# Performance work log

Hardware: AMD Instinct MI355X
Metric: run time of the kernel (lower is better)

The kernel has to match this reference:

```python
import jax, jax.numpy as jnp
import numpy as np

BETA = 0.25  # commitment loss weight


def setup_inputs() -> dict:
    key = jax.random.key(0)
    k1, k2 = jax.random.split(key)
    x = jax.random.normal(k1, (64, 64, 64, 64), dtype=jnp.float32)
    # embeddings: [embedding_dim=64, num_embeddings=512], random_uniform init in [-0.05, 0.05]
    embeddings = jax.random.uniform(k2, (64, 512), dtype=jnp.float32, minval=-0.05, maxval=0.05)
    return {"x": x, "embeddings": embeddings}


def reference(x, embeddings):
    d = embeddings.shape[0]
    flat = x.reshape(-1, d)                                   # [N, D]
    # squared L2 distances to each code: ||z||^2 + ||e||^2 - 2 z.e
    sim = flat @ embeddings                                   # [N, K]
    dist = (jnp.sum(flat * flat, axis=1, keepdims=True)
            + jnp.sum(embeddings * embeddings, axis=0)
            - 2.0 * sim)                                      # [N, K]
    idx = jnp.argmin(dist, axis=1)                            # [N]
    # gather nearest code (equivalent to one_hot @ embeddings.T)
    quantized = jnp.take(embeddings.T, idx, axis=0).reshape(x.shape)
    commitment_loss = jnp.mean((jax.lax.stop_gradient(quantized) - x) ** 2)
    codebook_loss = jnp.mean((quantized - jax.lax.stop_gradient(x)) ** 2)
    loss = BETA * commitment_loss + codebook_loss
    # straight-through estimator
    quantized_st = x + jax.lax.stop_gradient(quantized - x)
    return quantized_st, loss
```

## Files before the change

### kernel.cpp

```cpp
#include <hip/hip_runtime.h>


#define NROWS 262144
#define D 64
#define K 512
#define MARGIN 0.09f
#define INF32 3.4e38f

#define WS_ET 0
#define WS_E2 131072
#define WS_EBT 133120
#define WS_PARTIALS 198656

typedef __attribute__((ext_vector_type(8))) short bf16x8;
typedef __attribute__((ext_vector_type(4))) float f32x4;

union ClRed { unsigned cl[2048]; double red[256]; };

__device__ inline unsigned short f2bf(float f) {
    unsigned u = __float_as_uint(f);
    u += 0x7fffu + ((u >> 16) & 1u);
    return (unsigned short)(u >> 16);
}
__device__ inline unsigned pack_bf2(float lo, float hi) {
    unsigned ulo = __float_as_uint(lo); ulo += 0x7fffu + ((ulo >> 16) & 1u);
    unsigned uhi = __float_as_uint(hi); uhi += 0x7fffu + ((uhi >> 16) & 1u);
    return (ulo >> 16) | (uhi & 0xffff0000u);
}
__device__ inline bf16x8 pack8(float4 p, float4 q) {
    union { unsigned u[4]; bf16x8 v; } r;
    r.u[0] = pack_bf2(p.x, p.y); r.u[1] = pack_bf2(p.z, p.w);
    r.u[2] = pack_bf2(q.x, q.y); r.u[3] = pack_bf2(q.z, q.w);
    return r.v;
}

__global__ void __launch_bounds__(64) vq_prep(const float* __restrict__ emb, char* ws) {
    float* e2 = (float*)(ws + WS_E2);
    float* et = (float*)(ws + WS_ET);
    unsigned short* ebT = (unsigned short*)(ws + WS_EBT);
    int k = blockIdx.x * 64 + threadIdx.x;
    float v0 = emb[k];
    et[k * D] = v0;
    ebT[k * D] = f2bf(v0);
    float s = __fmul_rn(v0, v0);
    for (int d = 1; d < D; ++d) {
        float v = emb[d * K + k];
        et[k * D + d] = v;
        ebT[k * D + d] = f2bf(v);
        s = __fadd_rn(s, __fmul_rn(v, v));
    }
    e2[k] = s;
}

__device__ __noinline__ unsigned long long exact_pack(
        const float* __restrict__ x, const float* __restrict__ et,
        const float* __restrict__ e2f, int row, int k) {
    const float* xr = x + (size_t)row * D;
    float r0 = __fmul_rn(xr[0], xr[0]), r1 = __fmul_rn(xr[1], xr[1]);
    float r2 = __fmul_rn(xr[2], xr[2]), r3 = __fmul_rn(xr[3], xr[3]);
    float r4 = __fmul_rn(xr[4], xr[4]), r5 = __fmul_rn(xr[5], xr[5]);
    float r6 = __fmul_rn(xr[6], xr[6]), r7 = __fmul_rn(xr[7], xr[7]);
    for (int i = 8; i < 64; i += 8) {
        r0 = __fadd_rn(r0, __fmul_rn(xr[i],     xr[i]));
        r1 = __fadd_rn(r1, __fmul_rn(xr[i + 1], xr[i + 1]));
        r2 = __fadd_rn(r2, __fmul_rn(xr[i + 2], xr[i + 2]));
        r3 = __fadd_rn(r3, __fmul_rn(xr[i + 3], xr[i + 3]));
        r4 = __fadd_rn(r4, __fmul_rn(xr[i + 4], xr[i + 4]));
        r5 = __fadd_rn(r5, __fmul_rn(xr[i + 5], xr[i + 5]));
        r6 = __fadd_rn(r6, __fmul_rn(xr[i + 6], xr[i + 6]));
        r7 = __fadd_rn(r7, __fmul_rn(xr[i + 7], xr[i + 7]));
    }
    float z2 = __fadd_rn(__fadd_rn(__fadd_rn(r0, r1), __fadd_rn(r2, r3)),
                         __fadd_rn(__fadd_rn(r4, r5), __fadd_rn(r6, r7)));
    const float* ep = et + (size_t)k * D;
    float a = 0.f;
    for (int d = 0; d < D; ++d) a = fmaf(xr[d], ep[d], a);
    float dist = __fsub_rn(__fadd_rn(z2, e2f[k]), __fmul_rn(2.0f, a));
    return ((unsigned long long)__float_as_uint(dist) << 32) | (unsigned)k;
}

__global__ void __launch_bounds__(256) vq_fused(const float* __restrict__ x,
                                                float* __restrict__ out,
                                                char* __restrict__ ws) {
    const float* et  = (const float*)(ws + WS_ET);
    const float* e2f = (const float*)(ws + WS_E2);
    const unsigned short* ebT = (const unsigned short*)(ws + WS_EBT);
    double* partials = (double*)(ws + WS_PARTIALS);

    __shared__ unsigned short ebs[16384];
    __shared__ float le2[512];
    __shared__ unsigned long long lgmin[256];
    __shared__ int ccnt;
    __shared__ ClRed u;

    const int tid = threadIdx.x;
    const int wv = tid >> 6, lane = tid & 63;
    const int c15 = lane & 15;
    const int g = lane >> 4;
    const int kofs = g * 8;
    const int gr4 = g * 4;
    const int blockRow0 = blockIdx.x * 256;
    const int rowBase = blockRow0 + wv * 64;

    lgmin[tid] = 0xFFFFFFFFFFFFFFFFULL;
    if (tid == 0) ccnt = 0;
    le2[tid] = e2f[tid];
    le2[tid + 256] = e2f[tid + 256];

    bf16x8 aA0, aA1, aB0, aB1, aC0, aC1, aD0, aD1;
#define LOADA(RT, A0, A1) { \
    const float* xp = x + ((size_t)(rowBase + (RT) * 16 + c15)) * D + kofs; \
    float4 p0 = *(const float4*)xp; \
    float4 p1 = *(const float4*)(xp + 4); \
    float4 p2 = *(const float4*)(xp + 32); \
    float4 p3 = *(const float4*)(xp + 36); \
    A0 = pack8(p0, p1); A1 = pack8(p2, p3); }
    LOADA(0, aA0, aA1) LOADA(1, aB0, aB1) LOADA(2, aC0, aC1) LOADA(3, aD0, aD1)
#undef LOADA

#define STAGE(h) { \
    const uint4* src = (const uint4*)(ebT + (size_t)(h) * 16384); \
    _Pragma("unroll") \
    for (int i = 0; i < 8; ++i) { \
        int c = i * 256 + tid; \
        int kl = c >> 3, s = c & 7; \
        uint4 v = src[c]; \
        *(uint4*)(ebs + kl * 64 + ((s ^ (kl & 7)) * 8)) = v; \
    } }

#define SW1(A0, A1, M0, M1, M2, M3) { \
    f32x4 acc = {0.f, 0.f, 0.f, 0.f}; \
    acc = __builtin_amdgcn_mfma_f32_16x16x32_bf16(A0, bb0, acc, 0, 0, 0); \
    acc = __builtin_amdgcn_mfma_f32_16x16x32_bf16(A1, bb1, acc, 0, 0, 0); \
    M0 = fminf(M0, e2c - 2.0f * acc[0]); \
    M1 = fminf(M1, e2c - 2.0f * acc[1]); \
    M2 = fminf(M2, e2c - 2.0f * acc[2]); \
    M3 = fminf(M3, e2c - 2.0f * acc[3]); }

    float m00 = INF32, m01 = INF32, m02 = INF32, m03 = INF32;
    float m10 = INF32, m11 = INF32, m12 = INF32, m13 = INF32;
    float m20 = INF32, m21 = INF32, m22 = INF32, m23 = INF32;
    float m30 = INF32, m31 = INF32, m32 = INF32, m33 = INF32;

    for (int h = 0; h < 2; ++h) {
        __syncthreads();
        STAGE(h)
        __syncthreads();
        for (int j = 0; j < 16; ++j) {
            const int kkl = j * 16 + c15;
            bf16x8 bb0 = *(const bf16x8*)(ebs + kkl * 64 + ((g ^ (kkl & 7)) * 8));
            bf16x8 bb1 = *(const bf16x8*)(ebs + kkl * 64 + (((g + 4) ^ (kkl & 7)) * 8));
            float e2c = le2[h * 256 + kkl];
            SW1(aA0, aA1, m00, m01, m02, m03)
            SW1(aB0, aB1, m10, m11, m12, m13)
            SW1(aC0, aC1, m20, m21, m22, m23)
            SW1(aD0, aD1, m30, m31, m32, m33)
        }
    }
#undef SW1

#define RED(v) v = fminf(v, __shfl_xor(v, 1)); v = fminf(v, __shfl_xor(v, 2)); \
               v = fminf(v, __shfl_xor(v, 4)); v = fminf(v, __shfl_xor(v, 8)); \
               v += MARGIN;
    RED(m00) RED(m01) RED(m02) RED(m03)
    RED(m10) RED(m11) RED(m12) RED(m13)
    RED(m20) RED(m21) RED(m22) RED(m23)
    RED(m30) RED(m31) RED(m32) RED(m33)
#undef RED

#define PUSH(RT, R) { int idx = atomicAdd(&ccnt, 1); \
    if (idx < 2048) u.cl[idx] = \
        ((unsigned)(wv * 64 + (RT) * 16 + gr4 + (R)) << 16) | (unsigned)kg; \
    else atomicMin(&lgmin[wv * 64 + (RT) * 16 + gr4 + (R)], \
        exact_pack(x, et, e2f, blockRow0 + wv * 64 + (RT) * 16 + gr4 + (R), kg)); }

#define SW2(RT, A0, A1, M0, M1, M2, M3) { \
    f32x4 acc = {0.f, 0.f, 0.f, 0.f}; \
    acc = __builtin_amdgcn_mfma_f32_16x16x32_bf16(A0, bb0, acc, 0, 0, 0); \
    acc = __builtin_amdgcn_mfma_f32_16x16x32_bf16(A1, bb1, acc, 0, 0, 0); \
    if (e2c - 2.0f * acc[0] <= M0) PUSH(RT, 0) \
    if (e2c - 2.0f * acc[1] <= M1) PUSH(RT, 1) \
    if (e2c - 2.0f * acc[2] <= M2) PUSH(RT, 2) \
    if (e2c - 2.0f * acc[3] <= M3) PUSH(RT, 3) }

    for (int h = 0; h < 2; ++h) {
        __syncthreads();
        STAGE(h)
        __syncthreads();
        for (int j = 0; j < 16; ++j) {
            const int kkl = j * 16 + c15;
            const int kg = h * 256 + kkl;
            bf16x8 bb0 = *(const bf16x8*)(ebs + kkl * 64 + ((g ^ (kkl & 7)) * 8));
            bf16x8 bb1 = *(const bf16x8*)(ebs + kkl * 64 + (((g + 4) ^ (kkl & 7)) * 8));
            float e2c = le2[kg];
            SW2(0, aA0, aA1, m00, m01, m02, m03)
            SW2(1, aB0, aB1, m10, m11, m12, m13)
            SW2(2, aC0, aC1, m20, m21, m22, m23)
            SW2(3, aD0, aD1, m30, m31, m32, m33)
        }
    }
#undef SW2
#undef PUSH
#undef STAGE

    __syncthreads();
    const int cnt = (ccnt < 2048) ? ccnt : 2048;
    for (int i = tid; i < cnt; i += 256) {
        unsigned e = u.cl[i];
        int rowLocal = (int)(e >> 16);
        int k = (int)(e & 0x1ffu);
        atomicMin(&lgmin[rowLocal], exact_pack(x, et, e2f, blockRow0 + rowLocal, k));
    }
    __syncthreads();

    const int row = blockRow0 + tid;
    const int kb = (int)(lgmin[tid] & 0xFFFFFFFFULL);
    const float4* cq = (const float4*)(et + (size_t)kb * D);
    const float4* xr = (const float4*)(x + (size_t)row * D);
    float4* outr = (float4*)(out + (size_t)row * D);
    double rs = 0.0;
#define OUTQ(G) { \
        float4 e4 = cq[G]; float4 xv = xr[G]; float4 o; \
        float d0 = __fsub_rn(e4.x, xv.x); \
        float d1 = __fsub_rn(e4.y, xv.y); \
        float d2 = __fsub_rn(e4.z, xv.z); \
        float d3 = __fsub_rn(e4.w, xv.w); \
        o.x = __fadd_rn(xv.x, d0); \
        o.y = __fadd_rn(xv.y, d1); \
        o.z = __fadd_rn(xv.z, d2); \
        o.w = __fadd_rn(xv.w, d3); \
        outr[G] = o; \
        rs += (double)__fmul_rn(d0, d0) + (double)__fmul_rn(d1, d1) + \
              (double)__fmul_rn(d2, d2) + (double)__fmul_rn(d3, d3); }
    OUTQ(0) OUTQ(1) OUTQ(2) OUTQ(3) OUTQ(4) OUTQ(5) OUTQ(6) OUTQ(7)
    OUTQ(8) OUTQ(9) OUTQ(10) OUTQ(11) OUTQ(12) OUTQ(13) OUTQ(14) OUTQ(15)
#undef OUTQ

    u.red[tid] = rs;
    __syncthreads();
    for (int s = 128; s > 0; s >>= 1) {
        if (tid < s) u.red[tid] += u.red[tid + s];
        __syncthreads();
    }
    if (tid == 0) partials[blockIdx.x] = u.red[0];
}

__global__ void __launch_bounds__(256) vq_finalize(float* __restrict__ out, char* ws) {
    const double* partials = (const double*)(ws + WS_PARTIALS);
    __shared__ double red[256];
    double s = partials[threadIdx.x] + partials[threadIdx.x + 256] +
               partials[threadIdx.x + 512] + partials[threadIdx.x + 768];
    red[threadIdx.x] = s;
    __syncthreads();
    for (int st = 128; st > 0; st >>= 1) {
        if (threadIdx.x < st) red[threadIdx.x] += red[threadIdx.x + st];
        __syncthreads();
    }
    if (threadIdx.x == 0) {
        out[16777216] = (float)(1.25 * red[0] / 16777216.0);
    }
}

extern "C" void kernel_launch(void* const* d_in, const int* in_sizes, int n_in,
                              void* d_out, int out_size, void* d_ws, size_t ws_size,
                              hipStream_t stream) {
    const float* x   = (const float*)d_in[0];
    const float* emb = (const float*)d_in[1];
    float* out = (float*)d_out;
    char* ws = (char*)d_ws;

    vq_prep<<<8, 64, 0, stream>>>(emb, ws);
    vq_fused<<<NROWS / 256, 256, 0, stream>>>(x, out, ws);
    vq_finalize<<<1, 256, 0, stream>>>(out, ws);
}
```

Before: 183.7 us.

## Use single-wave blocks reading bf16 codebook directly from global/L2 instead of LDS staging

Shrinks the fused kernel from 256-thread to 64-thread blocks (one wavefront per block, 4096 blocks). The per-block LDS staging of the bf16 codebook and its barriers are removed, and each lane loads its B fragments straight from the global transposed codebook, relying on L1/L2 caching. The candidate list shrinks to 1024 entries and the loss partial sum becomes a shuffle reduction, with finalize summing 16 partials per thread. This removes LDS staging and block-wide syncs but adds global-memory latency to the inner MFMA loop, reads the codebook twice per wave, and increases the number of partials.

```diff
diff --git a/kernel.cpp b/kernel.cpp
--- a/kernel.cpp
+++ b/kernel.cpp
@@ -14,8 +14,6 @@
 
 typedef __attribute__((ext_vector_type(8))) short bf16x8;
 typedef __attribute__((ext_vector_type(4))) float f32x4;
-
-union ClRed { unsigned cl[2048]; double red[256]; };
 
 __device__ inline unsigned short f2bf(float f) {
     unsigned u = __float_as_uint(f);
@@ -79,33 +77,30 @@
     return ((unsigned long long)__float_as_uint(dist) << 32) | (unsigned)k;
 }
 
-__global__ void __launch_bounds__(256) vq_fused(const float* __restrict__ x,
-                                                float* __restrict__ out,
-                                                char* __restrict__ ws) {
+__global__ void __launch_bounds__(64, 4) vq_fused(const float* __restrict__ x,
+                                                  float* __restrict__ out,
+                                                  char* __restrict__ ws) {
     const float* et  = (const float*)(ws + WS_ET);
     const float* e2f = (const float*)(ws + WS_E2);
     const unsigned short* ebT = (const unsigned short*)(ws + WS_EBT);
     double* partials = (double*)(ws + WS_PARTIALS);
 
-    __shared__ unsigned short ebs[16384];
     __shared__ float le2[512];
-    __shared__ unsigned long long lgmin[256];
+    __shared__ unsigned long long lgmin[64];
+    __shared__ unsigned cl[1024];
     __shared__ int ccnt;
-    __shared__ ClRed u;
-
-    const int tid = threadIdx.x;
-    const int wv = tid >> 6, lane = tid & 63;
+
+    const int lane = threadIdx.x;
     const int c15 = lane & 15;
     const int g = lane >> 4;
     const int kofs = g * 8;
     const int gr4 = g * 4;
-    const int blockRow0 = blockIdx.x * 256;
-    const int rowBase = blockRow0 + wv * 64;
-
-    lgmin[tid] = 0xFFFFFFFFFFFFFFFFULL;
-    if (tid == 0) ccnt = 0;
-    le2[tid] = e2f[tid];
-    le2[tid + 256] = e2f[tid + 256];
+    const int rowBase = blockIdx.x * 64;
+
+    lgmin[lane] = 0xFFFFFFFFFFFFFFFFULL;
+    if (lane == 0) ccnt = 0;
+#pragma unroll
+    for (int i = 0; i < 8; ++i) le2[i * 64 + lane] = e2f[i * 64 + lane];
 
     bf16x8 aA0, aA1, aB0, aB1, aC0, aC1, aD0, aD1;
 #define LOADA(RT, A0, A1) { \
@@ -118,44 +113,32 @@
     LOADA(0, aA0, aA1) LOADA(1, aB0, aB1) LOADA(2, aC0, aC1) LOADA(3, aD0, aD1)
 #undef LOADA
 
-#define STAGE(h) { \
-    const uint4* src = (const uint4*)(ebT + (size_t)(h) * 16384); \
-    _Pragma("unroll") \
-    for (int i = 0; i < 8; ++i) { \
-        int c = i * 256 + tid; \
-        int kl = c >> 3, s = c & 7; \
-        uint4 v = src[c]; \
-        *(uint4*)(ebs + kl * 64 + ((s ^ (kl & 7)) * 8)) = v; \
-    } }
+    __syncthreads();
+
+    float m00 = INF32, m01 = INF32, m02 = INF32, m03 = INF32;
+    float m10 = INF32, m11 = INF32, m12 = INF32, m13 = INF32;
+    float m20 = INF32, m21 = INF32, m22 = INF32, m23 = INF32;
+    float m30 = INF32, m31 = INF32, m32 = INF32, m33 = INF32;
 
 #define SW1(A0, A1, M0, M1, M2, M3) { \
     f32x4 acc = {0.f, 0.f, 0.f, 0.f}; \
     acc = __builtin_amdgcn_mfma_f32_16x16x32_bf16(A0, bb0, acc, 0, 0, 0); \
     acc = __builtin_amdgcn_mfma_f32_16x16x32_bf16(A1, bb1, acc, 0, 0, 0); \
-    M0 = fminf(M0, e2c - 2.0f * acc[0]); \
-    M1 = fminf(M1, e2c - 2.0f * acc[1]); \
-    M2 = fminf(M2, e2c - 2.0f * acc[2]); \
-    M3 = fminf(M3, e2c - 2.0f * acc[3]); }
-
-    float m00 = INF32, m01 = INF32, m02 = INF32, m03 = INF32;
-    float m10 = INF32, m11 = INF32, m12 = INF32, m13 = INF32;
-    float m20 = INF32, m21 = INF32, m22 = INF32, m23 = INF32;
-    float m30 = INF32, m31 = INF32, m32 = INF32, m33 = INF32;
-
-    for (int h = 0; h < 2; ++h) {
-        __syncthreads();
-        STAGE(h)
-        __syncthreads();
-        for (int j = 0; j < 16; ++j) {
-            const int kkl = j * 16 + c15;
-            bf16x8 bb0 = *(const bf16x8*)(ebs + kkl * 64 + ((g ^ (kkl & 7)) * 8));
-            bf16x8 bb1 = *(const bf16x8*)(ebs + kkl * 64 + (((g + 4) ^ (kkl & 7)) * 8));
-            float e2c = le2[h * 256 + kkl];
-            SW1(aA0, aA1, m00, m01, m02, m03)
-            SW1(aB0, aB1, m10, m11, m12, m13)
-            SW1(aC0, aC1, m20, m21, m22, m23)
-            SW1(aD0, aD1, m30, m31, m32, m33)
-        }
+    M0 = fminf(M0, fmaf(-2.0f, acc[0], e2c)); \
+    M1 = fminf(M1, fmaf(-2.0f, acc[1], e2c)); \
+    M2 = fminf(M2, fmaf(-2.0f, acc[2], e2c)); \
+    M3 = fminf(M3, fmaf(-2.0f, acc[3], e2c)); }
+
+    for (int j = 0; j < 32; ++j) {
+        const int kkl = j * 16 + c15;
+        const unsigned short* bp = ebT + ((size_t)kkl << 6) + kofs;
+        bf16x8 bb0 = *(const bf16x8*)bp;
+        bf16x8 bb1 = *(const bf16x8*)(bp + 32);
+        float e2c = le2[kkl];
+        SW1(aA0, aA1, m00, m01, m02, m03)
+        SW1(aB0, aB1, m10, m11, m12, m13)
+        SW1(aC0, aC1, m20, m21, m22, m23)
+        SW1(aD0, aD1, m30, m31, m32, m33)
     }
 #undef SW1
 
@@ -169,52 +152,46 @@
 #undef RED
 
 #define PUSH(RT, R) { int idx = atomicAdd(&ccnt, 1); \
-    if (idx < 2048) u.cl[idx] = \
-        ((unsigned)(wv * 64 + (RT) * 16 + gr4 + (R)) << 16) | (unsigned)kg; \
-    else atomicMin(&lgmin[wv * 64 + (RT) * 16 + gr4 + (R)], \
-        exact_pack(x, et, e2f, blockRow0 + wv * 64 + (RT) * 16 + gr4 + (R), kg)); }
+    if (idx < 1024) cl[idx] = \
+        ((unsigned)((RT) * 16 + gr4 + (R)) << 9) | (unsigned)kkl; \
+    else atomicMin(&lgmin[(RT) * 16 + gr4 + (R)], \
+        exact_pack(x, et, e2f, rowBase + (RT) * 16 + gr4 + (R), kkl)); }
 
 #define SW2(RT, A0, A1, M0, M1, M2, M3) { \
     f32x4 acc = {0.f, 0.f, 0.f, 0.f}; \
     acc = __builtin_amdgcn_mfma_f32_16x16x32_bf16(A0, bb0, acc, 0, 0, 0); \
     acc = __builtin_amdgcn_mfma_f32_16x16x32_bf16(A1, bb1, acc, 0, 0, 0); \
-    if (e2c - 2.0f * acc[0] <= M0) PUSH(RT, 0) \
-    if (e2c - 2.0f * acc[1] <= M1) PUSH(RT, 1) \
-    if (e2c - 2.0f * acc[2] <= M2) PUSH(RT, 2) \
-    if (e2c - 2.0f * acc[3] <= M3) PUSH(RT, 3) }
-
-    for (int h = 0; h < 2; ++h) {
-        __syncthreads();
-        STAGE(h)
-        __syncthreads();
-        for (int j = 0; j < 16; ++j) {
-            const int kkl = j * 16 + c15;
-            const int kg = h * 256 + kkl;
-            bf16x8 bb0 = *(const bf16x8*)(ebs + kkl * 64 + ((g ^ (kkl & 7)) * 8));
-            bf16x8 bb1 = *(const bf16x8*)(ebs + kkl * 64 + (((g + 4) ^ (kkl & 7)) * 8));
-            float e2c = le2[kg];
-            SW2(0, aA0, aA1, m00, m01, m02, m03)
-            SW2(1, aB0, aB1, m10, m11, m12, m13)
-            SW2(2, aC0, aC1, m20, m21, m22, m23)
-            SW2(3, aD0, aD1, m30, m31, m32, m33)
-        }
+    if (fmaf(-2.0f, acc[0], e2c) <= M0) PUSH(RT, 0) \
+    if (fmaf(-2.0f, acc[1], e2c) <= M1) PUSH(RT, 1) \
+    if (fmaf(-2.0f, acc[2], e2c) <= M2) PUSH(RT, 2) \
+    if (fmaf(-2.0f, acc[3], e2c) <= M3) PUSH(RT, 3) }
+
+    for (int j = 0; j < 32; ++j) {
+        const int kkl = j * 16 + c15;
+        const unsigned short* bp = ebT + ((size_t)kkl << 6) + kofs;
+        bf16x8 bb0 = *(const bf16x8*)bp;
+        bf16x8 bb1 = *(const bf16x8*)(bp + 32);
+        float e2c = le2[kkl];
+        SW2(0, aA0, aA1, m00, m01, m02, m03)
+        SW2(1, aB0, aB1, m10, m11, m12, m13)
+        SW2(2, aC0, aC1, m20, m21, m22, m23)
+        SW2(3, aD0, aD1, m30, m31, m32, m33)
     }
 #undef SW2
 #undef PUSH
-#undef STAGE
-
-    __syncthreads();
-    const int cnt = (ccnt < 2048) ? ccnt : 2048;
-    for (int i = tid; i < cnt; i += 256) {
-        unsigned e = u.cl[i];
-        int rowLocal = (int)(e >> 16);
+
+    __syncthreads();
+    const int cnt = (ccnt < 1024) ? ccnt : 1024;
+    for (int i = lane; i < cnt; i += 64) {
+        unsigned e = cl[i];
+        int rowLocal = (int)(e >> 9);
         int k = (int)(e & 0x1ffu);
-        atomicMin(&lgmin[rowLocal], exact_pack(x, et, e2f, blockRow0 + rowLocal, k));
-    }
-    __syncthreads();
-
-    const int row = blockRow0 + tid;
-    const int kb = (int)(lgmin[tid] & 0xFFFFFFFFULL);
+        atomicMin(&lgmin[rowLocal], exact_pack(x, et, e2f, rowBase + rowLocal, k));
+    }
+    __syncthreads();
+
+    const int row = rowBase + lane;
+    const int kb = (int)(lgmin[lane] & 0xFFFFFFFFULL);
     const float4* cq = (const float4*)(et + (size_t)kb * D);
     const float4* xr = (const float4*)(x + (size_t)row * D);
     float4* outr = (float4*)(out + (size_t)row * D);
@@ -236,20 +213,17 @@
     OUTQ(8) OUTQ(9) OUTQ(10) OUTQ(11) OUTQ(12) OUTQ(13) OUTQ(14) OUTQ(15)
 #undef OUTQ
 
-    u.red[tid] = rs;
-    __syncthreads();
-    for (int s = 128; s > 0; s >>= 1) {
-        if (tid < s) u.red[tid] += u.red[tid + s];
-        __syncthreads();
-    }
-    if (tid == 0) partials[blockIdx.x] = u.red[0];
+#pragma unroll
+    for (int off = 32; off > 0; off >>= 1) rs += __shfl_down(rs, off);
+    if (lane == 0) partials[blockIdx.x] = rs;
 }
 
 __global__ void __launch_bounds__(256) vq_finalize(float* __restrict__ out, char* ws) {
     const double* partials = (const double*)(ws + WS_PARTIALS);
     __shared__ double red[256];
-    double s = partials[threadIdx.x] + partials[threadIdx.x + 256] +
-               partials[threadIdx.x + 512] + partials[threadIdx.x + 768];
+    double s = 0.0;
+#pragma unroll
+    for (int i = 0; i < 16; ++i) s += partials[threadIdx.x + 256 * i];
     red[threadIdx.x] = s;
     __syncthreads();
     for (int st = 128; st > 0; st >>= 1) {
@@ -270,6 +244,6 @@
     char* ws = (char*)d_ws;
 
     vq_prep<<<8, 64, 0, stream>>>(emb, ws);
-    vq_fused<<<NROWS / 256, 256, 0, stream>>>(x, out, ws);
+    vq_fused<<<NROWS / 64, 64, 0, stream>>>(x, out, ws);
     vq_finalize<<<1, 256, 0, stream>>>(out, ws);
 }
```

Measured after the change: 275.3 us. 49.9% more time.
